# Kernel optimization log

Measured on AMD Instinct MI355X. Metric: run time of the kernel, lower is better.

## Reference

```python
import jax, jax.numpy as jnp
import numpy as np

B, L, D, H, VOCAB = 8, 1024, 1024, 8, 32000
DH = D // H  # dim_per_head = 128
SCALE = float((DH // H) ** (-0.5))  # faithful to key.size(-1)//num_heads
EPS = 1e-5


def setup_inputs() -> dict:
    key = jax.random.key(0)
    ks = jax.random.split(key, 12)
    tokens = jax.random.randint(ks[0], (B, L), 0, VOCAB)
    s = 0.02
    emb = jax.random.normal(ks[1], (VOCAB, D), jnp.float32) * s
    emb = emb.at[0].set(0.0)  # padding_idx=0
    Wq = jax.random.normal(ks[2], (D, D), jnp.float32) * s
    Wk = jax.random.normal(ks[3], (D, D), jnp.float32) * s
    Wv = jax.random.normal(ks[4], (D, D), jnp.float32) * s
    Wo = jax.random.normal(ks[5], (D, D), jnp.float32) * s
    bq = jnp.zeros((D,), jnp.float32)
    bk = jnp.zeros((D,), jnp.float32)
    bv = jnp.zeros((D,), jnp.float32)
    bo = jnp.zeros((D,), jnp.float32)
    gamma = jnp.ones((2 * D,), jnp.float32)
    beta = jnp.zeros((2 * D,), jnp.float32)
    return {"tokens": tokens, "emb": emb, "Wq": Wq, "bq": bq, "Wk": Wk,
            "bk": bk, "Wv": Wv, "bv": bv, "Wo": Wo, "bo": bo,
            "gamma": gamma, "beta": beta}


def reference(tokens, emb, Wq, bq, Wk, bk, Wv, bv, Wo, bo, gamma, beta):
    # padding mask: [B, L, L] True where key token == 0
    pad = (tokens == 0)  # [B, L]
    mask = jnp.broadcast_to(pad[:, None, :], (B, L, L))
    mask = jnp.tile(mask, (H, 1, 1))  # torch .repeat(num_heads,1,1) -> [H*B, L, L]

    x = emb[tokens]  # [B, L, D]

    q = (x @ Wq + bq).reshape(B * H, L, DH)  # faithful interleaved view
    k = (x @ Wk + bk).reshape(B * H, L, DH)
    v = (x @ Wv + bv).reshape(B * H, L, DH)

    scores = jnp.einsum('bqd,bkd->bqk', q, k) * SCALE
    scores = jnp.where(mask, -jnp.inf, scores)
    attn = jax.nn.softmax(scores, axis=-1)
    ctx = jnp.einsum('bqk,bkd->bqd', attn, v).reshape(B, L, D)

    out = ctx @ Wo + bo  # [B, L, D]
    r = x + out
    maxpool = r.max(axis=1)   # [B, D]
    meanpool = r.mean(axis=1)  # [B, D]
    agg = jnp.concatenate([maxpool, meanpool], axis=1)  # [B, 2D]

    mu = agg.mean(axis=-1, keepdims=True)
    var = agg.var(axis=-1, keepdims=True)
    return (agg - mu) / jnp.sqrt(var + EPS) * gamma + beta
```

## Files before the change

kernel.cpp:

```cpp
#include <hip/hip_runtime.h>
#include <math.h>

typedef __attribute__((ext_vector_type(8))) short short8;
typedef __attribute__((ext_vector_type(4))) float f32x4;

constexpr int CB = 8, CL = 1024, CD = 1024, CDH = 128, CM = 8192;
constexpr float CSCALE = 0.25f;
constexpr float CEPS = 1e-5f;

__device__ inline ushort f2b(float f) {
    union { float f; unsigned u; } v; v.f = f;
    unsigned r = v.u + 0x7FFF + ((v.u >> 16) & 1);
    return (ushort)(r >> 16);
}
__device__ inline float b2f(ushort u) {
    union { unsigned u; float f; } v; v.u = ((unsigned)u) << 16;
    return v.f;
}

__device__ inline void gld16(const void* g, void* l) {
    __builtin_amdgcn_global_load_lds(
        (const __attribute__((address_space(1))) void*)g,
        (__attribute__((address_space(3))) void*)l, 16, 0, 0);
}

__global__ __launch_bounds__(256) void k_gather(const int* __restrict__ tokens,
                                                const float* __restrict__ emb,
                                                float* __restrict__ x,
                                                ushort* __restrict__ xb) {
    int row = blockIdx.x;
    int tok = tokens[row];
    float4 v = ((const float4*)(emb + (size_t)tok * CD))[threadIdx.x];
    ((float4*)(x + (size_t)row * CD))[threadIdx.x] = v;
    ushort4 o; o.x = f2b(v.x); o.y = f2b(v.y); o.z = f2b(v.z); o.w = f2b(v.w);
    ((ushort4*)(xb + (size_t)row * CD))[threadIdx.x] = o;
}

__global__ __launch_bounds__(256) void k_wtrans(const float* __restrict__ W,
                                                ushort* __restrict__ Wt) {
    __shared__ float ws_[32][33];
    const int tk = blockIdx.x * 32, tn = blockIdx.y * 32;
    const int t = threadIdx.x;
    {
        int r = t >> 3, c4 = (t & 7) * 4;
        *(float4*)&ws_[r][c4] = *(const float4*)&W[(size_t)(tk + r) * CD + tn + c4];
    }
    __syncthreads();
    int n = t >> 3, k4 = (t & 7) * 4;
    ushort4 o;
    o.x = f2b(ws_[k4 + 0][n]); o.y = f2b(ws_[k4 + 1][n]);
    o.z = f2b(ws_[k4 + 2][n]); o.w = f2b(ws_[k4 + 3][n]);
    *(ushort4*)&Wt[(size_t)(tn + n) * CD + tk + k4] = o;
}

__global__ __launch_bounds__(256) void k_gemm_qkv(const ushort* __restrict__ A,
                                                  const ushort* __restrict__ Wt3,
                                                  const float* __restrict__ b0,
                                                  const float* __restrict__ b1,
                                                  const float* __restrict__ b2,
                                                  ushort* __restrict__ C3) {
    __shared__ ushort As[128 * 32];
    __shared__ ushort Bs[128 * 32];
    const int z = blockIdx.z;
    const ushort* Bt  = Wt3 + (size_t)z * CD * CD;
    const float* bias = (z == 0) ? b0 : ((z == 1) ? b1 : b2);
    ushort* Cout      = C3 + (size_t)z * CM * CD;

    const int t = threadIdx.x, w = t >> 6, l = t & 63;
    const int lane15 = l & 15, quad = l >> 4;
    const int bm = blockIdx.y * 128, bn = blockIdx.x * 128;
    const int wm = (w >> 1) * 64, wn = (w & 1) * 64;
    const int arow = l >> 2;
    const int aseg = (l & 3) * 8;
    f32x4 acc[4][4] = {};

    for (int k0 = 0; k0 < CD; k0 += 32) {
        __syncthreads();
        #pragma unroll
        for (int c2 = 0; c2 < 2; ++c2) {
            int c = w * 2 + c2;
            gld16(A  + (size_t)(bm + c * 16 + arow) * CD + k0 + aseg, &As[c * 512 + l * 8]);
            gld16(Bt + (size_t)(bn + c * 16 + arow) * CD + k0 + aseg, &Bs[c * 512 + l * 8]);
        }
        __syncthreads();
        short8 af[4], bf[4];
        #pragma unroll
        for (int im = 0; im < 4; ++im)
            af[im] = *(const short8*)&As[(wm + im * 16 + lane15) * 32 + quad * 8];
        #pragma unroll
        for (int in = 0; in < 4; ++in)
            bf[in] = *(const short8*)&Bs[(wn + in * 16 + lane15) * 32 + quad * 8];
        #pragma unroll
        for (int im = 0; im < 4; ++im)
            #pragma unroll
            for (int in = 0; in < 4; ++in)
                acc[im][in] = __builtin_amdgcn_mfma_f32_16x16x32_bf16(af[im], bf[in], acc[im][in], 0, 0, 0);
    }
    #pragma unroll
    for (int in = 0; in < 4; ++in) {
        int col = bn + wn + in * 16 + lane15;
        float bv = bias[col];
        #pragma unroll
        for (int im = 0; im < 4; ++im) {
            int row0 = bm + wm + im * 16 + quad * 4;
            #pragma unroll
            for (int r = 0; r < 4; ++r)
                Cout[(size_t)(row0 + r) * CD + col] = f2b(acc[im][in][r] + bv);
        }
    }
}

__global__ __launch_bounds__(256) void k_gemm_out(const ushort* __restrict__ A,
                                                  const ushort* __restrict__ Bt,
                                                  const float* __restrict__ bias,
                                                  const float* __restrict__ resid,
                                                  float* __restrict__ pmax,
                                                  float* __restrict__ psum) {
    __shared__ ushort As[128 * 32];
    __shared__ ushort Bs[128 * 32];
    __shared__ float redmx[4][64], redsm[4][64];
    const int t = threadIdx.x, w = t >> 6, l = t & 63;
    const int lane15 = l & 15, quad = l >> 4;
    const int bm = blockIdx.y * 128, bn = blockIdx.x * 128;
    const int wm = (w >> 1) * 64, wn = (w & 1) * 64;
    const int arow = l >> 2;
    const int aseg = (l & 3) * 8;
    f32x4 acc[4][4] = {};

    for (int k0 = 0; k0 < CD; k0 += 32) {
        __syncthreads();
        #pragma unroll
        for (int c2 = 0; c2 < 2; ++c2) {
            int c = w * 2 + c2;
            gld16(A  + (size_t)(bm + c * 16 + arow) * CD + k0 + aseg, &As[c * 512 + l * 8]);
            gld16(Bt + (size_t)(bn + c * 16 + arow) * CD + k0 + aseg, &Bs[c * 512 + l * 8]);
        }
        __syncthreads();
        short8 af[4], bf[4];
        #pragma unroll
        for (int im = 0; im < 4; ++im)
            af[im] = *(const short8*)&As[(wm + im * 16 + lane15) * 32 + quad * 8];
        #pragma unroll
        for (int in = 0; in < 4; ++in)
            bf[in] = *(const short8*)&Bs[(wn + in * 16 + lane15) * 32 + quad * 8];
        #pragma unroll
        for (int im = 0; im < 4; ++im)
            #pragma unroll
            for (int in = 0; in < 4; ++in)
                acc[im][in] = __builtin_amdgcn_mfma_f32_16x16x32_bf16(af[im], bf[in], acc[im][in], 0, 0, 0);
    }
    const int by = blockIdx.y, bb = by >> 3, chunk = by & 7;
    float vmax_[4], vsum_[4];
    #pragma unroll
    for (int in = 0; in < 4; ++in) {
        int col = bn + wn + in * 16 + lane15;
        float bvv = bias[col];
        float mx = -3.4e38f, sm = 0.f;
        #pragma unroll
        for (int im = 0; im < 4; ++im) {
            int row0 = bm + wm + im * 16 + quad * 4;
            #pragma unroll
            for (int r = 0; r < 4; ++r) {
                float rel = acc[im][in][r] + bvv + resid[(size_t)(row0 + r) * CD + col];
                mx = fmaxf(mx, rel);
                sm += rel;
            }
        }
        mx = fmaxf(mx, __shfl_xor(mx, 16));
        mx = fmaxf(mx, __shfl_xor(mx, 32));
        sm += __shfl_xor(sm, 16);
        sm += __shfl_xor(sm, 32);
        vmax_[in] = mx; vsum_[in] = sm;
    }
    if (l < 16) {
        #pragma unroll
        for (int in = 0; in < 4; ++in) {
            redmx[w][in * 16 + lane15] = vmax_[in];
            redsm[w][in * 16 + lane15] = vsum_[in];
        }
    }
    __syncthreads();
    if (t < 128) {
        int wcol = t >> 6, cc = t & 63;
        float m = fmaxf(redmx[wcol][cc], redmx[wcol + 2][cc]);
        float s = redsm[wcol][cc] + redsm[wcol + 2][cc];
        size_t off2 = ((size_t)bb * 8 + chunk) * CD + bn + wcol * 64 + cc;
        pmax[off2] = m;
        psum[off2] = s;
    }
}

__global__ __launch_bounds__(256) void k_vtransp(const ushort* __restrict__ v,
                                                 ushort* __restrict__ Vtp) {
    __shared__ ushort Vs[64 * 136];
    const int i = blockIdx.x >> 4, kt = blockIdx.x & 15;
    const ushort* src = v + (size_t)i * 131072 + (size_t)kt * 64 * 128;
    const int t = threadIdx.x;
    #pragma unroll
    for (int ii = 0; ii < 4; ++ii) {
        int idx = t + 256 * ii;
        int key = idx >> 4, seg = idx & 15;
        *(uint4*)&Vs[key * 136 + seg * 8] = *(const uint4*)&src[key * 128 + seg * 8];
    }
    __syncthreads();
    ushort* dst = Vtp + (size_t)blockIdx.x * 8192;
    #pragma unroll
    for (int it = 0; it < 4; ++it) {
        int L = t + 256 * it;
        int cell = L & 63;
        int quadk = cell >> 4, l15 = cell & 15;
        int p = L >> 6;
        int d = (p >> 1) * 16 + l15;
        int kb = ((p & 1) * 4 + quadk) * 8;
        uint pk[4];
        #pragma unroll
        for (int jj = 0; jj < 4; ++jj) {
            uint lo = Vs[(kb + 2 * jj) * 136 + d];
            uint hi = Vs[(kb + 2 * jj + 1) * 136 + d];
            pk[jj] = lo | (hi << 16);
        }
        *(uint4*)&dst[(size_t)L * 8] = *(uint4*)pk;
    }
}

__device__ inline void attn_stage(const ushort* __restrict__ K,
                                  const ushort* __restrict__ Vtp,
                                  ushort* KsBuf, ushort* VsBuf,
                                  int i, int kt, int w, int l,
                                  int lane15, int quad) {
    #pragma unroll
    for (int c = 0; c < 4; ++c) {
        int p = w * 4 + c;
        gld16(K + (size_t)i * 131072 + (size_t)(kt * 64 + (p >> 2) * 16 + lane15) * 128
                + (p & 3) * 32 + quad * 8,
              KsBuf + p * 512 + (size_t)l * 8);
        gld16(Vtp + ((size_t)(i * 16 + kt) * 16 + p) * 512 + (size_t)l * 8,
              VsBuf + p * 512 + (size_t)l * 8);
    }
}

__global__ __launch_bounds__(256) void k_attn(const ushort* __restrict__ Q,
                                              const ushort* __restrict__ K,
                                              const ushort* __restrict__ Vtp,
                                              const int* __restrict__ tokens,
                                              ushort* __restrict__ ctx) {
    __shared__ ushort Ks[2][16 * 512];
    __shared__ ushort Vs[2][16 * 512];
    __shared__ ushort Ps[4 * 1088];
    __shared__ ushort Msk[CL];
    const int i = blockIdx.x, qb = blockIdx.y * 128;
    const int t = threadIdx.x, w = t >> 6, l = t & 63;
    const int lane15 = l & 15, quad = l >> 4;

    {
        const int* tokb = tokens + (i & 7) * CL;
        #pragma unroll
        for (int jj = 0; jj < 4; ++jj) {
            int idx = t + 256 * jj;
            Msk[idx] = (tokb[idx] == 0) ? (ushort)0xFF80 : (ushort)0;
        }
    }
    short8 af[2][4];
    #pragma unroll
    for (int g = 0; g < 2; ++g)
        #pragma unroll
        for (int kc = 0; kc < 4; ++kc)
            af[g][kc] = *(const short8*)&Q[(size_t)i * 131072
                + (size_t)(qb + w * 32 + g * 16 + lane15) * 128 + kc * 32 + quad * 8];

    f32x4 oacc[2][8];
    #pragma unroll
    for (int g = 0; g < 2; ++g)
        #pragma unroll
        for (int dt = 0; dt < 8; ++dt) oacc[g][dt] = f32x4{0.f, 0.f, 0.f, 0.f};
    float lsum[2][4] = {};
    const int wbase = w * 1088;

    attn_stage(K, Vtp, Ks[0], Vs[0], i, 0, w, l, lane15, quad);
    __syncthreads();

    for (int kt = 0; kt < 16; ++kt) {
        const int cur = kt & 1;
        if (kt < 15)
            attn_stage(K, Vtp, Ks[cur ^ 1], Vs[cur ^ 1], i, kt + 1, w, l, lane15, quad);

        f32x4 sc[2][4];
        #pragma unroll
        for (int j = 0; j < 4; ++j) {
            short8 bk[4];
            #pragma unroll
            for (int kc = 0; kc < 4; ++kc)
                bk[kc] = *(const short8*)&Ks[cur][(j * 4 + kc) * 512 + l * 8];
            #pragma unroll
            for (int g = 0; g < 2; ++g) {
                sc[g][j] = f32x4{0.f, 0.f, 0.f, 0.f};
                #pragma unroll
                for (int kc = 0; kc < 4; ++kc)
                    sc[g][j] = __builtin_amdgcn_mfma_f32_16x16x32_bf16(af[g][kc], bk[kc], sc[g][j], 0, 0, 0);
            }
        }
        #pragma unroll
        for (int j = 0; j < 4; ++j) {
            float mj = b2f(Msk[kt * 64 + j * 16 + lane15]);
            #pragma unroll
            for (int g = 0; g < 2; ++g)
                #pragma unroll
                for (int r = 0; r < 4; ++r) {
                    float pv = __expf(fmaf(sc[g][j][r], CSCALE, mj));
                    sc[g][j][r] = pv;
                    lsum[g][r] += pv;
                }
        }
        short8 ap[2][2];
        #pragma unroll
        for (int g = 0; g < 2; ++g) {
            #pragma unroll
            for (int j = 0; j < 4; ++j) {
                int ks2 = j >> 1;
                int qq  = (j & 1) * 2 + (lane15 >> 3);
                int pos = lane15 & 7;
                #pragma unroll
                for (int r = 0; r < 4; ++r) {
                    union { float f; unsigned u; } cv; cv.f = sc[g][j][r];
                    Ps[wbase + ks2 * 544 + qq * 136 + (quad * 4 + r) * 8 + pos] =
                        (ushort)(cv.u >> 16);
                }
            }
            #pragma unroll
            for (int ks2 = 0; ks2 < 2; ++ks2)
                ap[g][ks2] = *(const short8*)&Ps[wbase + ks2 * 544 + quad * 136 + lane15 * 8];
        }
        #pragma unroll
        for (int dt = 0; dt < 8; ++dt)
            #pragma unroll
            for (int ks2 = 0; ks2 < 2; ++ks2) {
                short8 bv = *(const short8*)&Vs[cur][(dt * 2 + ks2) * 512 + l * 8];
                #pragma unroll
                for (int g = 0; g < 2; ++g)
                    oacc[g][dt] = __builtin_amdgcn_mfma_f32_16x16x32_bf16(ap[g][ks2], bv, oacc[g][dt], 0, 0, 0);
            }
        __syncthreads();
    }
    #pragma unroll
    for (int g = 0; g < 2; ++g) {
        float inv[4];
        #pragma unroll
        for (int r = 0; r < 4; ++r) {
            float s = lsum[g][r];
            #pragma unroll
            for (int off = 1; off < 16; off <<= 1) s += __shfl_xor(s, off);
            inv[r] = 1.f / s;
        }
        #pragma unroll
        for (int dt = 0; dt < 8; ++dt)
            #pragma unroll
            for (int r = 0; r < 4; ++r) {
                int q = qb + w * 32 + g * 16 + quad * 4 + r;
                ctx[(size_t)i * 131072 + (size_t)q * 128 + dt * 16 + lane15] =
                    f2b(oacc[g][dt][r] * inv[r]);
            }
    }
}

__global__ __launch_bounds__(1024) void k_pool2(const float* __restrict__ pmax,
                                                const float* __restrict__ psum,
                                                const float* __restrict__ gamma,
                                                const float* __restrict__ beta,
                                                float* __restrict__ out) {
    __shared__ float rs[16], rq[16];
    __shared__ float s_mu, s_inv;
    const int b = blockIdx.x;
    const int d = threadIdx.x;
    float mx = -3.4e38f, sm = 0.f;
    #pragma unroll
    for (int c = 0; c < 8; ++c) {
        size_t off = ((size_t)b * 8 + c) * CD + d;
        mx = fmaxf(mx, pmax[off]);
        sm += psum[off];
    }
    const float a0 = mx;
    const float a1 = sm * (1.0f / 1024.0f);
    float s = a0 + a1;
    float qd = a0 * a0 + a1 * a1;
    #pragma unroll
    for (int off = 32; off > 0; off >>= 1) {
        s  += __shfl_xor(s, off);
        qd += __shfl_xor(qd, off);
    }
    const int wid = d >> 6;
    if ((d & 63) == 0) { rs[wid] = s; rq[wid] = qd; }
    __syncthreads();
    if (d == 0) {
        float S = 0.f, Qm = 0.f;
        for (int ww = 0; ww < 16; ++ww) { S += rs[ww]; Qm += rq[ww]; }
        float mu  = S * (1.0f / 2048.0f);
        float var = Qm * (1.0f / 2048.0f) - mu * mu;
        s_mu = mu; s_inv = 1.0f / sqrtf(var + CEPS);
    }
    __syncthreads();
    const float mu = s_mu, inv = s_inv;
    out[(size_t)b * 2048 + d]        = (a0 - mu) * inv * gamma[d]        + beta[d];
    out[(size_t)b * 2048 + 1024 + d] = (a1 - mu) * inv * gamma[1024 + d] + beta[1024 + d];
}

extern "C" void kernel_launch(void* const* d_in, const int* in_sizes, int n_in,
                              void* d_out, int out_size, void* d_ws, size_t ws_size,
                              hipStream_t stream) {
    const int*   tokens = (const int*)d_in[0];
    const float* emb    = (const float*)d_in[1];
    const float* Wq     = (const float*)d_in[2];
    const float* bq     = (const float*)d_in[3];
    const float* Wk     = (const float*)d_in[4];
    const float* bk     = (const float*)d_in[5];
    const float* Wv     = (const float*)d_in[6];
    const float* bv     = (const float*)d_in[7];
    const float* Wo     = (const float*)d_in[8];
    const float* bo     = (const float*)d_in[9];
    const float* gamma  = (const float*)d_in[10];
    const float* beta   = (const float*)d_in[11];
    float* out = (float*)d_out;

    char* p = (char*)d_ws;
    float*  x   = (float*)p;   p += (size_t)CM * CD * 4;
    ushort* xb  = (ushort*)p;  p += (size_t)CM * CD * 2;
    ushort* wqt = (ushort*)p;  p += (size_t)CD * CD * 2;
    ushort* wkt = (ushort*)p;  p += (size_t)CD * CD * 2;
    ushort* wvt = (ushort*)p;  p += (size_t)CD * CD * 2;
    ushort* wot = (ushort*)p;  p += (size_t)CD * CD * 2;
    ushort* qb_ = (ushort*)p;  p += (size_t)CM * CD * 2;
    ushort* kb_ = (ushort*)p;  p += (size_t)CM * CD * 2;
    ushort* vb_ = (ushort*)p;  p += (size_t)CM * CD * 2;
    ushort* Vtp = (ushort*)p;  p += (size_t)CM * CD * 2;
    float*  pmax = (float*)p;  p += (size_t)CB * 8 * CD * 4;
    float*  psum = (float*)p;  p += (size_t)CB * 8 * CD * 4;
    ushort* ctx = vb_;

    k_gather<<<CM, 256, 0, stream>>>(tokens, emb, x, xb);

    dim3 wg(32, 32);
    k_wtrans<<<wg, 256, 0, stream>>>(Wq, wqt);
    k_wtrans<<<wg, 256, 0, stream>>>(Wk, wkt);
    k_wtrans<<<wg, 256, 0, stream>>>(Wv, wvt);
    k_wtrans<<<wg, 256, 0, stream>>>(Wo, wot);

    dim3 gq(CD / 128, CM / 128, 3);
    k_gemm_qkv<<<gq, 256, 0, stream>>>(xb, wqt, bq, bk, bv, qb_);

    k_vtransp<<<64 * 16, 256, 0, stream>>>(vb_, Vtp);

    dim3 ag(64, 8);
    k_attn<<<ag, 256, 0, stream>>>(qb_, kb_, Vtp, tokens, ctx);

    dim3 go(CD / 128, CM / 128);
    k_gemm_out<<<go, 256, 0, stream>>>(ctx, wot, bo, x, pmax, psum);

    k_pool2<<<CB, 1024, 0, stream>>>(pmax, psum, gamma, beta, out);
}
```

Before: 366.8 us.

## Batch weight transposes, swizzle GEMM block order, raise MFMA priority in attention

Merges the four weight-transpose launches into one launch that picks the weight matrix by blockIdx.z, relying on the contiguous workspace layout of the transposed weights. Remaps GEMM block indices so that consecutive blocks cover 8 column tiles of the same row band, improving L2 reuse of the A operand. Wraps the attention MFMA sections in s_setprio to favour matrix issue over other waves. The aim is less launch overhead and better cache locality, at the cost of changed scheduling behaviour.

```diff
diff --git a/kernel.cpp b/kernel.cpp
--- a/kernel.cpp
+++ b/kernel.cpp
@@ -36,9 +36,15 @@
     ((ushort4*)(xb + (size_t)row * CD))[threadIdx.x] = o;
 }
 
-__global__ __launch_bounds__(256) void k_wtrans(const float* __restrict__ W,
+__global__ __launch_bounds__(256) void k_wtrans(const float* __restrict__ W0,
+                                                const float* __restrict__ W1,
+                                                const float* __restrict__ W2,
+                                                const float* __restrict__ W3,
                                                 ushort* __restrict__ Wt) {
     __shared__ float ws_[32][33];
+    const int z = blockIdx.z;
+    const float* W = (z == 0) ? W0 : ((z == 1) ? W1 : ((z == 2) ? W2 : W3));
+    ushort* Wtz = Wt + (size_t)z * CD * CD;
     const int tk = blockIdx.x * 32, tn = blockIdx.y * 32;
     const int t = threadIdx.x;
     {
@@ -50,7 +56,7 @@
     ushort4 o;
     o.x = f2b(ws_[k4 + 0][n]); o.y = f2b(ws_[k4 + 1][n]);
     o.z = f2b(ws_[k4 + 2][n]); o.w = f2b(ws_[k4 + 3][n]);
-    *(ushort4*)&Wt[(size_t)(tn + n) * CD + tk + k4] = o;
+    *(ushort4*)&Wtz[(size_t)(tn + n) * CD + tk + k4] = o;
 }
 
 __global__ __launch_bounds__(256) void k_gemm_qkv(const ushort* __restrict__ A,
@@ -68,7 +74,8 @@
 
     const int t = threadIdx.x, w = t >> 6, l = t & 63;
     const int lane15 = l & 15, quad = l >> 4;
-    const int bm = blockIdx.y * 128, bn = blockIdx.x * 128;
+    const int bm = (blockIdx.x * 8 + (blockIdx.y >> 3)) * 128;
+    const int bn = (blockIdx.y & 7) * 128;
     const int wm = (w >> 1) * 64, wn = (w & 1) * 64;
     const int arow = l >> 2;
     const int aseg = (l & 3) * 8;
@@ -121,7 +128,8 @@
     __shared__ float redmx[4][64], redsm[4][64];
     const int t = threadIdx.x, w = t >> 6, l = t & 63;
     const int lane15 = l & 15, quad = l >> 4;
-    const int bm = blockIdx.y * 128, bn = blockIdx.x * 128;
+    const int bm = (blockIdx.x * 8 + (blockIdx.y >> 3)) * 128;
+    const int bn = (blockIdx.y & 7) * 128;
     const int wm = (w >> 1) * 64, wn = (w & 1) * 64;
     const int arow = l >> 2;
     const int aseg = (l & 3) * 8;
@@ -149,7 +157,7 @@
             for (int in = 0; in < 4; ++in)
                 acc[im][in] = __builtin_amdgcn_mfma_f32_16x16x32_bf16(af[im], bf[in], acc[im][in], 0, 0, 0);
     }
-    const int by = blockIdx.y, bb = by >> 3, chunk = by & 7;
+    const int by = bm >> 7, bb = by >> 3, chunk = by & 7;
     float vmax_[4], vsum_[4];
     #pragma unroll
     for (int in = 0; in < 4; ++in) {
@@ -285,6 +293,7 @@
             attn_stage(K, Vtp, Ks[cur ^ 1], Vs[cur ^ 1], i, kt + 1, w, l, lane15, quad);
 
         f32x4 sc[2][4];
+        __builtin_amdgcn_s_setprio(1);
         #pragma unroll
         for (int j = 0; j < 4; ++j) {
             short8 bk[4];
@@ -299,6 +308,7 @@
                     sc[g][j] = __builtin_amdgcn_mfma_f32_16x16x32_bf16(af[g][kc], bk[kc], sc[g][j], 0, 0, 0);
             }
         }
+        __builtin_amdgcn_s_setprio(0);
         #pragma unroll
         for (int j = 0; j < 4; ++j) {
             float mj = b2f(Msk[kt * 64 + j * 16 + lane15]);
@@ -330,6 +340,7 @@
             for (int ks2 = 0; ks2 < 2; ++ks2)
                 ap[g][ks2] = *(const short8*)&Ps[wbase + ks2 * 544 + quad * 136 + lane15 * 8];
         }
+        __builtin_amdgcn_s_setprio(1);
         #pragma unroll
         for (int dt = 0; dt < 8; ++dt)
             #pragma unroll
@@ -339,6 +350,7 @@
                 for (int g = 0; g < 2; ++g)
                     oacc[g][dt] = __builtin_amdgcn_mfma_f32_16x16x32_bf16(ap[g][ks2], bv, oacc[g][dt], 0, 0, 0);
             }
+        __builtin_amdgcn_s_setprio(0);
         __syncthreads();
     }
     #pragma unroll
@@ -434,14 +446,12 @@
     float*  pmax = (float*)p;  p += (size_t)CB * 8 * CD * 4;
     float*  psum = (float*)p;  p += (size_t)CB * 8 * CD * 4;
     ushort* ctx = vb_;
+    (void)wkt; (void)wvt;
 
     k_gather<<<CM, 256, 0, stream>>>(tokens, emb, x, xb);
 
-    dim3 wg(32, 32);
-    k_wtrans<<<wg, 256, 0, stream>>>(Wq, wqt);
-    k_wtrans<<<wg, 256, 0, stream>>>(Wk, wkt);
-    k_wtrans<<<wg, 256, 0, stream>>>(Wv, wvt);
-    k_wtrans<<<wg, 256, 0, stream>>>(Wo, wot);
+    dim3 wg(32, 32, 4);
+    k_wtrans<<<wg, 256, 0, stream>>>(Wq, Wk, Wv, Wo, wqt);
 
     dim3 gq(CD / 128, CM / 128, 3);
     k_gemm_qkv<<<gq, 256, 0, stream>>>(xb, wqt, bq, bk, bv, qb_);
```

After: 351.5 us. 1.04x faster.
